# Optimization experiments

Measured on AMD Instinct MI355X. Metric: run time of the kernel, lower is better.

## Reference

```python
import jax, jax.numpy as jnp
import numpy as np

EPSILON = 1e-15
CUTOFF = 5.0
N_RBF = 16           # num_radial_filters -> RBF dim = 2*16+1 = 33
SCALE = 8            # _quadrature_points_per_atom_scaling


def poly_envelope_5_2(x):
    # e3nn.poly_envelope(5, 2): f'(x) ~ x^5 (1-x)^2, f(0)=1, f(1)=0
    x2 = x * x
    x6 = x2 * x2 * x2
    f = 1.0 - 28.0 * x6 + 48.0 * x6 * x - 21.0 * x6 * x2
    return jnp.where(x < 1.0, f, jnp.zeros_like(x))


def sin_cos_basis(r, n_rbf):
    r = r[..., None]                                  # [A,T,1]
    k = jnp.arange(1, n_rbf + 1, dtype=r.dtype)       # [n_rbf]
    return jnp.sqrt(2.0) * jnp.concatenate(
        [0.1 * jnp.ones_like(r), jnp.sin(k * jnp.pi * r), jnp.cos(k * jnp.pi * r)],
        axis=-1,
    )                                                 # [A,T,2*n_rbf+1]


def spherical_harmonics_l012_norm(d):
    # Real spherical harmonics up to l=2, e3nn m-ordering, normalization='norm'
    # (each l-block has unit norm for unit input directions).
    x, y, z = d[..., 0], d[..., 1], d[..., 2]
    r2 = x * x + y * y + z * z
    s3 = jnp.sqrt(3.0)
    one = jnp.ones_like(x)
    return jnp.stack(
        [
            one,                       # l=0
            y, z, x,                   # l=1 (m=-1,0,1)
            s3 * x * y,                # l=2 m=-2
            s3 * y * z,                # l=2 m=-1
            0.5 * (3.0 * z * z - r2),  # l=2 m=0
            s3 * x * z,                # l=2 m=1
            0.5 * s3 * (x * x - y * y) # l=2 m=2
        ],
        axis=-1,
    )                                  # [A,T,9]


def setup_inputs() -> dict:
    key = jax.random.key(0)
    k1, k2, k3, k4 = jax.random.split(key, 4)
    A, N = 64, 200000
    nuc_pos = 4.0 * jax.random.normal(k1, (A, 3), dtype=jnp.float32)
    grid_coords = 4.0 * jax.random.normal(k2, (N, 3), dtype=jnp.float32)
    weights = jax.random.uniform(k3, (N,), dtype=jnp.float32)
    n = jax.random.uniform(k4, (N,), dtype=jnp.float32)
    atom_mask = jnp.ones((A,), dtype=bool)
    return {"nuc_pos": nuc_pos, "atom_mask": atom_mask,
            "grid_coords": grid_coords, "weights": weights, "n": n}


def reference(nuc_pos, atom_mask, grid_coords, weights, n):
    g = grid_coords / CUTOFF                          # [N,3]
    p = nuc_pos / CUTOFF                              # [A,3]
    diff = p[:, None] - g[None]                       # [A,N,3]
    dist = jnp.linalg.norm(diff, axis=-1)             # [A,N]
    A, N = dist.shape
    T = min(N, SCALE * N // A)                        # static
    idx = jnp.argsort(dist, axis=1)[:, :T]            # [A,T] nearest grid points
    diff = jnp.take_along_axis(diff, idx[:, :, None], axis=1)   # [A,T,3]
    dist = jnp.take_along_axis(dist, idx, axis=1)                # [A,T]
    n_t = n[idx]                                      # [A,T]
    w_t = weights[idx]                                # [A,T]
    rbf = sin_cos_basis(dist, N_RBF) * poly_envelope_5_2(dist)[..., None]  # [A,T,33]
    dirs = diff / (dist[..., None] + EPSILON)         # [A,T,3]
    sh = spherical_harmonics_l012_norm(dirs)          # [A,T,9]
    node_feats = jnp.einsum('atr,ath,at,at->arh', rbf, sh, n_t, w_t)  # [A,33,9]
    return node_feats
```

## Files before the change

### kernel.cpp

```cpp
#include <hip/hip_runtime.h>
#include <hip/hip_fp16.h>


typedef float f32x4 __attribute__((ext_vector_type(4)));
typedef int   i32x4 __attribute__((ext_vector_type(4)));

#define SLICES 32
#define NB1    256
#define NB2    512
#define CLAMP0 4000u
#define CHA    1
#define NCHUNK (SLICES * CHA)
#define PBSTR  304
#define CUT25  0x41C80000u
#define WROWS  49
#define BBASE  (33 * 72)

__device__ __forceinline__ unsigned short tobf(float v) {
  return (unsigned short)((__float_as_uint(v) + 0x8000u) >> 16);
}

__device__ __forceinline__ unsigned pack2h(float a, float b) {
  __half2 h = __floats2half2_rn(a, b);
  return *reinterpret_cast<unsigned*>(&h);
}

__device__ __forceinline__ void mfma_acc(f32x4& d, i32x4 a, i32x4 b) {
  asm("v_mfma_f32_16x16x32_bf16 %0, %1, %2, %0" : "+v"(d) : "v"(a), "v"(b));
}

__global__ __launch_bounds__(256) void enc_hist_store(
    const float* __restrict__ nuc, const float* __restrict__ grid,
    const float* __restrict__ wv, const float* __restrict__ nv, int N,
    unsigned* __restrict__ hists, unsigned* __restrict__ cnt,
    unsigned* __restrict__ bitsArr, uint2* __restrict__ pay, int scap,
    unsigned* __restrict__ ghist2) {
  __shared__ unsigned lh[NB1];
  __shared__ unsigned s_cnt;
  int a = blockIdx.x / SLICES, s = blockIdx.x % SLICES;
  int tid = threadIdx.x, lane = tid & 63;
  if (tid < NB1) lh[tid] = 0;
  if (tid == 0) s_cnt = 0;
  {
    const int stripe = NB2 / SLICES;
    if (tid < stripe) ghist2[(size_t)a * NB2 + s * stripe + tid] = 0;
  }
  __syncthreads();

  float px = nuc[3*a+0], py = nuc[3*a+1], pz = nuc[3*a+2];
  unsigned* segb = bitsArr + (size_t)blockIdx.x * scap;
  uint2*    segp = pay     + (size_t)blockIdx.x * scap;
  const float4* G4 = (const float4*)grid;
  const float4* W4 = (const float4*)wv;
  const float4* V4 = (const float4*)nv;
  int nq = N >> 2;
  int qper = (nq + SLICES - 1) / SLICES;
  int qlo = s * qper, qhi = min(nq, qlo + qper);

  for (int qi = qlo + tid; qi < qhi; qi += 256) {
    float4 A4 = G4[3*qi], B4 = G4[3*qi+1], C4 = G4[3*qi+2];
    float4 w4 = W4[qi], v4 = V4[qi];
    float xs[4] = {A4.x, A4.w, B4.z, C4.y};
    float ys[4] = {A4.y, B4.x, B4.w, C4.z};
    float zs[4] = {A4.z, B4.y, C4.x, C4.w};
    float nws[4] = {v4.x * w4.x, v4.y * w4.y, v4.z * w4.z, v4.w * w4.w};
    float dxs[4], dys[4], dzs[4];
    unsigned bt[4];
    #pragma unroll
    for (int k = 0; k < 4; ++k) {
      float dx = px - xs[k], dy = py - ys[k], dz = pz - zs[k];
      dxs[k] = dx; dys[k] = dy; dzs[k] = dz;
      float d2 = __fmaf_rn(dx, dx, __fmaf_rn(dy, dy, __fmul_rn(dz, dz)));
      bt[k] = __float_as_uint(d2);
      if (bt[k] < CUT25) {
        int cb = (int)(bt[k] >> 18) - (int)CLAMP0;
        atomicAdd(&lh[cb > 0 ? cb : 0], 1u);
      }
    }
    #pragma unroll
    for (int k = 0; k < 4; ++k) {
      bool sel = bt[k] < CUT25;
      unsigned long long mm = __ballot(sel);
      if (mm) {
        int leader = __ffsll(mm) - 1;
        unsigned base = 0;
        if (lane == leader) base = atomicAdd(&s_cnt, (unsigned)__popcll(mm));
        base = __shfl(base, leader);
        if (sel) {
          unsigned pos = base + (unsigned)__popcll(mm & ((1ull << lane) - 1ull));
          if (pos < (unsigned)scap) {
            segb[pos] = bt[k];
            segp[pos] = make_uint2(pack2h(dxs[k], dys[k]), pack2h(dzs[k], nws[k]));
          }
        }
      }
    }
  }
  if (s == SLICES - 1) {
    for (int i = 4*nq + tid; i < N; i += 256) {
      float dx = px - grid[3*i+0], dy = py - grid[3*i+1], dz = pz - grid[3*i+2];
      float d2 = __fmaf_rn(dx, dx, __fmaf_rn(dy, dy, __fmul_rn(dz, dz)));
      unsigned bits = __float_as_uint(d2);
      bool sel = bits < CUT25;
      if (sel) {
        int cb = (int)(bits >> 18) - (int)CLAMP0;
        atomicAdd(&lh[cb > 0 ? cb : 0], 1u);
      }
      unsigned long long mm = __ballot(sel);
      if (mm) {
        int leader = __ffsll(mm) - 1;
        unsigned base = 0;
        if (lane == leader) base = atomicAdd(&s_cnt, (unsigned)__popcll(mm));
        base = __shfl(base, leader);
        if (sel) {
          unsigned pos = base + (unsigned)__popcll(mm & ((1ull << lane) - 1ull));
          if (pos < (unsigned)scap) {
            segb[pos] = bits;
            segp[pos] = make_uint2(pack2h(dx, dy), pack2h(dz, nv[i] * wv[i]));
          }
        }
      }
    }
  }
  __syncthreads();
  if (tid < NB1) hists[(size_t)blockIdx.x * NB1 + tid] = lh[tid];
  if (tid == 0) cnt[blockIdx.x] = s_cnt;
}

__global__ __launch_bounds__(256) void enc_scan1(
    const unsigned* __restrict__ hists, unsigned T,
    unsigned* __restrict__ b1r, unsigned* __restrict__ r2r) {
  __shared__ unsigned lh[NB1];
  __shared__ unsigned s_bin, s_pre;
  int a = blockIdx.x, tid = threadIdx.x;
  if (tid < NB1) {
    unsigned acc = 0;
    const unsigned* base = hists + (size_t)a * SLICES * NB1 + tid;
    #pragma unroll 8
    for (int t = 0; t < SLICES; ++t) acc += base[(size_t)t * NB1];
    lh[tid] = acc;
  }
  if (tid == 0) { s_bin = NB1 - 1; s_pre = 0; }
  __syncthreads();
  if (tid < 64) {
    int lane = tid, base = 4 * lane;
    unsigned h0 = lh[base], h1 = lh[base+1], h2 = lh[base+2], h3 = lh[base+3];
    unsigned ssum = h0 + h1 + h2 + h3;
    unsigned p = ssum;
    #pragma unroll
    for (int d = 1; d < 64; d <<= 1) {
      unsigned t = __shfl_up(p, d);
      if (lane >= d) p += t;
    }
    unsigned excl = p - ssum;
    if (excl < T && T <= p) {
      unsigned cum = excl;
      unsigned hh[4] = {h0, h1, h2, h3};
      #pragma unroll
      for (int k = 0; k < 4; ++k) {
        if (cum + hh[k] >= T) { s_bin = (unsigned)(base + k); s_pre = cum; break; }
        cum += hh[k];
      }
    }
  }
  __syncthreads();
  if (tid == 0) { b1r[a] = s_bin; r2r[a] = T - s_pre; }
}

__global__ __launch_bounds__(256) void enc_fine(
    const unsigned* __restrict__ b1r, const unsigned* __restrict__ cnt,
    const unsigned* __restrict__ bitsArr, int scap,
    unsigned* __restrict__ ghist2) {
  int seg_id = blockIdx.x;
  int a = seg_id / SLICES;
  unsigned b1c = b1r[a];
  unsigned tb1 = b1c + CLAMP0;
  int total = min((int)cnt[seg_id], scap);
  const unsigned* segb = bitsArr + (size_t)seg_id * scap;
  unsigned* gh2 = ghist2 + (size_t)a * NB2;
  for (int i = threadIdx.x; i < total; i += 256) {
    unsigned bits = segb[i];
    unsigned cb = bits >> 18;
    bool match = b1c ? (cb == tb1) : (cb <= CLAMP0);
    if (match) atomicAdd(&gh2[(bits >> 9) & (NB2 - 1)], 1u);
  }
}

__global__ __launch_bounds__(256) void enc_scan2(
    const unsigned* __restrict__ ghist2, const unsigned* __restrict__ b1r,
    const unsigned* __restrict__ r2r, unsigned* __restrict__ thr) {
  __shared__ unsigned lh2[NB2];
  __shared__ unsigned s_bin2;
  int a = blockIdx.x, tid = threadIdx.x;
  const unsigned* gh2 = ghist2 + (size_t)a * NB2;
  lh2[tid] = gh2[tid];
  lh2[tid + 256] = gh2[tid + 256];
  if (tid == 0) s_bin2 = NB2 - 1;
  __syncthreads();
  unsigned R = r2r[a];
  if (tid < 64) {
    int lane = tid, base = 8 * lane;
    unsigned hh[8], ssum = 0;
    #pragma unroll
    for (int k = 0; k < 8; ++k) { hh[k] = lh2[base + k]; ssum += hh[k]; }
    unsigned p = ssum;
    #pragma unroll
    for (int d = 1; d < 64; d <<= 1) {
      unsigned t = __shfl_up(p, d);
      if (lane >= d) p += t;
    }
    unsigned excl = p - ssum;
    if (excl < R && R <= p) {
      unsigned cum = excl;
      #pragma unroll
      for (int k = 0; k < 8; ++k) {
        if (cum + hh[k] >= R) { s_bin2 = (unsigned)(base + k); break; }
        cum += hh[k];
      }
    }
  }
  __syncthreads();
  if (tid == 0) thr[a] = ((b1r[a] + CLAMP0) << 9) | s_bin2;
}

__global__ __launch_bounds__(256, 5) void enc_accum(
    const unsigned* __restrict__ thrv, const unsigned* __restrict__ cnt,
    const unsigned* __restrict__ bitsArr, const uint2* __restrict__ pay,
    int scap, float* __restrict__ pb) {
  __shared__ __align__(16) unsigned short lds[4][WROWS * 72];
  int seg_id = blockIdx.x;
  int a = seg_id / SLICES;
  int tid = threadIdx.x, lane = tid & 63, w = tid >> 6;
  unsigned short* SB = &lds[w][0];

  {
    i32x4 z = {0, 0, 0, 0};
    i32x4* zp = (i32x4*)SB;
    #pragma unroll
    for (int t = 0; t < 7; ++t) {
      int idx = lane + t * 64;
      if (idx < (WROWS * 72) / 8) zp[idx] = z;
    }
  }

  unsigned thr = thrv[a];
  int total = min((int)cnt[seg_id], scap);
  const unsigned* lstb = bitsArr + (size_t)seg_id * scap;
  const uint2*    lstp = pay     + (size_t)seg_id * scap;

  f32x4 acc0 = {0,0,0,0}, acc1 = {0,0,0,0}, acc2 = {0,0,0,0};
  int m = lane & 15, q = lane >> 4;
  const float SQRT2 = 1.41421356237309515f;
  const float PIF   = 3.14159265358979323846f;
  const float S3    = 1.73205080756887729f;

  int j0 = w * 64 + lane;
  unsigned bitsN = (j0 < total) ? lstb[j0] : 0xFFFFFFFFu;
  uint2 prN = make_uint2(0u, 0u);
  if (j0 < total) prN = lstp[j0];

  for (int jb = w * 64; jb < total; jb += 256) {
    unsigned bits = bitsN;
    uint2 pr = prN;
    int jn = jb + 256 + lane;
    if (jn < total) { bitsN = lstb[jn]; prN = lstp[jn]; }
    bool live = (jb + lane < total) && ((bits >> 9) <= thr);
    if (live) {
      float d2 = __uint_as_float(bits);
      __half2 hxy = *reinterpret_cast<const __half2*>(&pr.x);
      __half2 hzn = *reinterpret_cast<const __half2*>(&pr.y);
      float dx = __low2float(hxy), dy = __high2float(hxy);
      float dz = __low2float(hzn), nw = __high2float(hzn);
#if __has_builtin(__builtin_amdgcn_sqrtf)
      float rn = __builtin_amdgcn_sqrtf(d2) * 0.2f;
#else
      float rn = sqrtf(d2) * 0.2f;
#endif
      float x2 = rn * rn;
      float x6 = x2 * x2 * x2;
      float e  = __fmaf_rn(x6, __fmaf_rn(-21.f, x2, __fmaf_rn(48.f, rn, -28.f)), 1.f);
      float f  = SQRT2 * e;
#if __has_builtin(__builtin_amdgcn_rcpf)
      float inv = 0.2f * __builtin_amdgcn_rcpf(rn + 1e-15f);
#else
      float inv = 0.2f / (rn + 1e-15f);
#endif
      float X = dx * inv, Y = dy * inv, Z = dz * inv;
      float r2 = __fmaf_rn(X, X, __fmaf_rn(Y, Y, Z * Z));
      SB[BBASE + 0*72 + lane] = tobf(nw);
      SB[BBASE + 1*72 + lane] = tobf(nw * Y);
      SB[BBASE + 2*72 + lane] = tobf(nw * Z);
      SB[BBASE + 3*72 + lane] = tobf(nw * X);
      SB[BBASE + 4*72 + lane] = tobf(nw * S3 * X * Y);
      SB[BBASE + 5*72 + lane] = tobf(nw * S3 * Y * Z);
      SB[BBASE + 6*72 + lane] = tobf(nw * 0.5f * __fmaf_rn(3.f, Z * Z, -r2));
      SB[BBASE + 7*72 + lane] = tobf(nw * S3 * X * Z);
      SB[BBASE + 8*72 + lane] = tobf(nw * 0.5f * S3 * (X * X - Y * Y));
      float s1, c1;
      __sincosf(PIF * rn, &s1, &c1);
      SB[0 * 72 + lane]  = tobf(0.1f * f);
      float sk = s1, ck = c1;
      SB[1 * 72 + lane]  = tobf(f * sk);
      SB[17 * 72 + lane] = tobf(f * ck);
      #pragma unroll
      for (int k = 2; k <= 16; ++k) {
        float sn = __fmaf_rn(sk, c1, ck * s1);
        float cn = __fmaf_rn(ck, c1, -(sk * s1));
        sk = sn; ck = cn;
        SB[k * 72 + lane]        = tobf(f * sk);
        SB[(16 + k) * 72 + lane] = tobf(f * ck);
      }
    } else {
      #pragma unroll
      for (int h = 0; h < 9; ++h) SB[BBASE + h * 72 + lane] = 0;
    }
    #pragma unroll
    for (int g = 0; g < 2; ++g) {
      int cb = 8 * q + 32 * g;
      i32x4 bf = *(const i32x4*)&SB[BBASE + m * 72 + cb];
      i32x4 a0 = *(const i32x4*)&SB[(0  + m) * 72 + cb];
      mfma_acc(acc0, a0, bf);
      i32x4 a1 = *(const i32x4*)&SB[(16 + m) * 72 + cb];
      mfma_acc(acc1, a1, bf);
      i32x4 a2 = *(const i32x4*)&SB[(32 + m) * 72 + cb];
      mfma_acc(acc2, a2, bf);
    }
  }
  asm volatile("s_nop 7\n\ts_nop 7" : "+v"(acc0), "+v"(acc1), "+v"(acc2));

  float* redw = (float*)&lds[w][0];
  if (m < 9) {
    #pragma unroll
    for (int t = 0; t < 4; ++t) {
      int row = 4 * q + t;
      redw[(row +  0) * 9 + m] = acc0[t];
      redw[(row + 16) * 9 + m] = acc1[t];
      if (row + 32 < 33) redw[(row + 32) * 9 + m] = acc2[t];
    }
  }
  __syncthreads();
  float* pbb = pb + (size_t)blockIdx.x * PBSTR;
  for (int v = tid; v < 297; v += 256) {
    float s0 = ((const float*)&lds[0][0])[v] + ((const float*)&lds[1][0])[v];
    float s1 = ((const float*)&lds[2][0])[v] + ((const float*)&lds[3][0])[v];
    pbb[v] = s0 + s1;
  }
}

__global__ __launch_bounds__(256) void enc_reduce(
    const float* __restrict__ pb, float* __restrict__ out, int nout) {
  int idx = blockIdx.x * 256 + threadIdx.x;
  if (idx >= nout) return;
  int a = idx / 297, v = idx - a * 297;
  const float* p = pb + (size_t)a * NCHUNK * PBSTR + v;
  float s = 0.f;
  #pragma unroll 8
  for (int k = 0; k < NCHUNK; ++k) s += p[(size_t)k * PBSTR];
  out[idx] = s;
}

extern "C" void kernel_launch(void* const* d_in, const int* in_sizes, int n_in,
                              void* d_out, int out_size, void* d_ws, size_t ws_size,
                              hipStream_t stream) {
  const float* nuc  = (const float*)d_in[0];
  const float* grid = (const float*)d_in[2];
  const float* wts  = (const float*)d_in[3];
  const float* nn   = (const float*)d_in[4];
  int A = in_sizes[0] / 3;
  int N = in_sizes[2] / 3;
  long long t8 = (8LL * (long long)N) / (long long)A;
  unsigned T = (unsigned)(t8 < (long long)N ? t8 : (long long)N);

  unsigned* ws      = (unsigned*)d_ws;
  unsigned* cnt     = ws;
  unsigned* b1r     = cnt + A * SLICES;
  unsigned* r2r     = b1r + A;
  unsigned* thr     = r2r + A;
  unsigned* hists   = thr + A;
  unsigned* ghist2  = hists + (size_t)A * SLICES * NB1;
  float*    pb      = (float*)(ghist2 + (size_t)A * NB2);
  unsigned* bitsArr = (unsigned*)(pb + (size_t)A * SLICES * CHA * PBSTR);

  int nq   = N >> 2;
  int qper = (nq + SLICES - 1) / SLICES;
  int SCAP = qper * 4 + 4;
  {
    long long head  = (long long)(bitsArr - ws);
    long long avail = (long long)(ws_size / 4) - head;
    long long need  = 3LL * SCAP * A * SLICES;
    if (avail > 0 && need > avail) SCAP = (int)(avail / (3LL * A * SLICES));
    SCAP &= ~1;
  }
  uint2* pay = (uint2*)(bitsArr + (size_t)A * SLICES * SCAP);
  float* out = (float*)d_out;
  int nout = A * 297;

  enc_hist_store<<<A * SLICES,         256, 0, stream>>>(nuc, grid, wts, nn, N, hists,
                                                         cnt, bitsArr, pay, SCAP, ghist2);
  enc_scan1     <<<A,                  256, 0, stream>>>(hists, T, b1r, r2r);
  enc_fine      <<<A * SLICES,         256, 0, stream>>>(b1r, cnt, bitsArr, SCAP, ghist2);
  enc_scan2     <<<A,                  256, 0, stream>>>(ghist2, b1r, r2r, thr);
  enc_accum     <<<A * SLICES * CHA,   256, 0, stream>>>(thr, cnt, bitsArr, pay, SCAP, pb);
  enc_reduce    <<<(nout + 255) / 256, 256, 0, stream>>>(pb, out, nout);
}
```

Before: 57.52 us.

## Process four atoms per block in histogram/store pass to reuse grid loads

After: 65.57 us. 14.0% more time.

```diff
diff --git a/kernel.cpp b/kernel.cpp
--- a/kernel.cpp
+++ b/kernel.cpp
@@ -6,11 +6,11 @@
 typedef int   i32x4 __attribute__((ext_vector_type(4)));
 
 #define SLICES 32
+#define AG     4
 #define NB1    256
 #define NB2    512
 #define CLAMP0 4000u
-#define CHA    1
-#define NCHUNK (SLICES * CHA)
+#define NCHUNK SLICES
 #define PBSTR  304
 #define CUT25  0x41C80000u
 #define WROWS  49
@@ -35,21 +35,41 @@
     unsigned* __restrict__ hists, unsigned* __restrict__ cnt,
     unsigned* __restrict__ bitsArr, uint2* __restrict__ pay, int scap,
     unsigned* __restrict__ ghist2) {
-  __shared__ unsigned lh[NB1];
-  __shared__ unsigned s_cnt;
-  int a = blockIdx.x / SLICES, s = blockIdx.x % SLICES;
+  __shared__ unsigned lh[AG][NB1];
+  __shared__ unsigned s_cnt[AG];
+  int ag = blockIdx.x / SLICES, s = blockIdx.x % SLICES;
+  int a0 = ag * AG;
   int tid = threadIdx.x, lane = tid & 63;
-  if (tid < NB1) lh[tid] = 0;
-  if (tid == 0) s_cnt = 0;
+  if (tid < NB1) {
+    #pragma unroll
+    for (int aa = 0; aa < AG; ++aa) lh[aa][tid] = 0;
+  }
+  if (tid < AG) s_cnt[tid] = 0;
   {
     const int stripe = NB2 / SLICES;
-    if (tid < stripe) ghist2[(size_t)a * NB2 + s * stripe + tid] = 0;
-  }
-  __syncthreads();
-
-  float px = nuc[3*a+0], py = nuc[3*a+1], pz = nuc[3*a+2];
-  unsigned* segb = bitsArr + (size_t)blockIdx.x * scap;
-  uint2*    segp = pay     + (size_t)blockIdx.x * scap;
+    if (tid < stripe) {
+      #pragma unroll
+      for (int aa = 0; aa < AG; ++aa)
+        ghist2[(size_t)(a0 + aa) * NB2 + s * stripe + tid] = 0;
+    }
+  }
+  __syncthreads();
+
+  float pxs[AG], pys[AG], pzs[AG];
+  #pragma unroll
+  for (int aa = 0; aa < AG; ++aa) {
+    pxs[aa] = nuc[3*(a0+aa)+0];
+    pys[aa] = nuc[3*(a0+aa)+1];
+    pzs[aa] = nuc[3*(a0+aa)+2];
+  }
+  unsigned* segb[AG];
+  uint2*    segp[AG];
+  #pragma unroll
+  for (int aa = 0; aa < AG; ++aa) {
+    size_t off = (size_t)((a0 + aa) * SLICES + s) * scap;
+    segb[aa] = bitsArr + off;
+    segp[aa] = pay + off;
+  }
   const float4* G4 = (const float4*)grid;
   const float4* W4 = (const float4*)wv;
   const float4* V4 = (const float4*)nv;
@@ -64,33 +84,38 @@
     float ys[4] = {A4.y, B4.x, B4.w, C4.z};
     float zs[4] = {A4.z, B4.y, C4.x, C4.w};
     float nws[4] = {v4.x * w4.x, v4.y * w4.y, v4.z * w4.z, v4.w * w4.w};
-    float dxs[4], dys[4], dzs[4];
-    unsigned bt[4];
-    #pragma unroll
-    for (int k = 0; k < 4; ++k) {
-      float dx = px - xs[k], dy = py - ys[k], dz = pz - zs[k];
-      dxs[k] = dx; dys[k] = dy; dzs[k] = dz;
-      float d2 = __fmaf_rn(dx, dx, __fmaf_rn(dy, dy, __fmul_rn(dz, dz)));
-      bt[k] = __float_as_uint(d2);
-      if (bt[k] < CUT25) {
-        int cb = (int)(bt[k] >> 18) - (int)CLAMP0;
-        atomicAdd(&lh[cb > 0 ? cb : 0], 1u);
-      }
-    }
-    #pragma unroll
-    for (int k = 0; k < 4; ++k) {
-      bool sel = bt[k] < CUT25;
-      unsigned long long mm = __ballot(sel);
-      if (mm) {
-        int leader = __ffsll(mm) - 1;
-        unsigned base = 0;
-        if (lane == leader) base = atomicAdd(&s_cnt, (unsigned)__popcll(mm));
-        base = __shfl(base, leader);
-        if (sel) {
-          unsigned pos = base + (unsigned)__popcll(mm & ((1ull << lane) - 1ull));
-          if (pos < (unsigned)scap) {
-            segb[pos] = bt[k];
-            segp[pos] = make_uint2(pack2h(dxs[k], dys[k]), pack2h(dzs[k], nws[k]));
+    #pragma unroll
+    for (int aa = 0; aa < AG; ++aa) {
+      float px = pxs[aa], py = pys[aa], pz = pzs[aa];
+      float dxs[4], dys[4], dzs[4];
+      unsigned bt[4];
+      #pragma unroll
+      for (int k = 0; k < 4; ++k) {
+        float dx = px - xs[k], dy = py - ys[k], dz = pz - zs[k];
+        dxs[k] = dx; dys[k] = dy; dzs[k] = dz;
+        float d2 = __fmaf_rn(dx, dx, __fmaf_rn(dy, dy, __fmul_rn(dz, dz)));
+        bt[k] = __float_as_uint(d2);
+        if (bt[k] < CUT25) {
+          int cb = (int)(bt[k] >> 18) - (int)CLAMP0;
+          atomicAdd(&lh[aa][cb > 0 ? cb : 0], 1u);
+        }
+      }
+      #pragma unroll
+      for (int k = 0; k < 4; ++k) {
+        bool sel = bt[k] < CUT25;
+        unsigned long long mm = __ballot(sel);
+        if (mm) {
+          int leader = __ffsll(mm) - 1;
+          unsigned base = 0;
+          if (lane == leader) base = atomicAdd(&s_cnt[aa], (unsigned)__popcll(mm));
+          base = __shfl(base, leader);
+          if (sel) {
+            unsigned pos = base + (unsigned)__popcll(mm & ((1ull << lane) - 1ull));
+            if (pos < (unsigned)scap) {
+              segb[aa][pos] = bt[k];
+              segp[aa][pos] = make_uint2(pack2h(dxs[k], dys[k]),
+                                         pack2h(dzs[k], nws[k]));
+            }
           }
         }
       }
@@ -98,33 +123,42 @@
   }
   if (s == SLICES - 1) {
     for (int i = 4*nq + tid; i < N; i += 256) {
-      float dx = px - grid[3*i+0], dy = py - grid[3*i+1], dz = pz - grid[3*i+2];
-      float d2 = __fmaf_rn(dx, dx, __fmaf_rn(dy, dy, __fmul_rn(dz, dz)));
-      unsigned bits = __float_as_uint(d2);
-      bool sel = bits < CUT25;
-      if (sel) {
-        int cb = (int)(bits >> 18) - (int)CLAMP0;
-        atomicAdd(&lh[cb > 0 ? cb : 0], 1u);
-      }
-      unsigned long long mm = __ballot(sel);
-      if (mm) {
-        int leader = __ffsll(mm) - 1;
-        unsigned base = 0;
-        if (lane == leader) base = atomicAdd(&s_cnt, (unsigned)__popcll(mm));
-        base = __shfl(base, leader);
+      float gx = grid[3*i+0], gy = grid[3*i+1], gz = grid[3*i+2];
+      float nwi = nv[i] * wv[i];
+      #pragma unroll
+      for (int aa = 0; aa < AG; ++aa) {
+        float dx = pxs[aa] - gx, dy = pys[aa] - gy, dz = pzs[aa] - gz;
+        float d2 = __fmaf_rn(dx, dx, __fmaf_rn(dy, dy, __fmul_rn(dz, dz)));
+        unsigned bits = __float_as_uint(d2);
+        bool sel = bits < CUT25;
         if (sel) {
-          unsigned pos = base + (unsigned)__popcll(mm & ((1ull << lane) - 1ull));
-          if (pos < (unsigned)scap) {
-            segb[pos] = bits;
-            segp[pos] = make_uint2(pack2h(dx, dy), pack2h(dz, nv[i] * wv[i]));
+          int cb = (int)(bits >> 18) - (int)CLAMP0;
+          atomicAdd(&lh[aa][cb > 0 ? cb : 0], 1u);
+        }
+        unsigned long long mm = __ballot(sel);
+        if (mm) {
+          int leader = __ffsll(mm) - 1;
+          unsigned base = 0;
+          if (lane == leader) base = atomicAdd(&s_cnt[aa], (unsigned)__popcll(mm));
+          base = __shfl(base, leader);
+          if (sel) {
+            unsigned pos = base + (unsigned)__popcll(mm & ((1ull << lane) - 1ull));
+            if (pos < (unsigned)scap) {
+              segb[aa][pos] = bits;
+              segp[aa][pos] = make_uint2(pack2h(dx, dy), pack2h(dz, nwi));
+            }
           }
         }
       }
     }
   }
   __syncthreads();
-  if (tid < NB1) hists[(size_t)blockIdx.x * NB1 + tid] = lh[tid];
-  if (tid == 0) cnt[blockIdx.x] = s_cnt;
+  if (tid < NB1) {
+    #pragma unroll
+    for (int aa = 0; aa < AG; ++aa)
+      hists[(size_t)((a0 + aa) * SLICES + s) * NB1 + tid] = lh[aa][tid];
+  }
+  if (tid < AG) cnt[(a0 + tid) * SLICES + s] = s_cnt[tid];
 }
 
 __global__ __launch_bounds__(256) void enc_scan1(
@@ -379,7 +413,7 @@
   unsigned* hists   = thr + A;
   unsigned* ghist2  = hists + (size_t)A * SLICES * NB1;
   float*    pb      = (float*)(ghist2 + (size_t)A * NB2);
-  unsigned* bitsArr = (unsigned*)(pb + (size_t)A * SLICES * CHA * PBSTR);
+  unsigned* bitsArr = (unsigned*)(pb + (size_t)A * NCHUNK * PBSTR);
 
   int nq   = N >> 2;
   int qper = (nq + SLICES - 1) / SLICES;
@@ -395,11 +429,11 @@
   float* out = (float*)d_out;
   int nout = A * 297;
 
-  enc_hist_store<<<A * SLICES,         256, 0, stream>>>(nuc, grid, wts, nn, N, hists,
+  enc_hist_store<<<(A / AG) * SLICES,  256, 0, stream>>>(nuc, grid, wts, nn, N, hists,
                                                          cnt, bitsArr, pay, SCAP, ghist2);
   enc_scan1     <<<A,                  256, 0, stream>>>(hists, T, b1r, r2r);
   enc_fine      <<<A * SLICES,         256, 0, stream>>>(b1r, cnt, bitsArr, SCAP, ghist2);
   enc_scan2     <<<A,                  256, 0, stream>>>(ghist2, b1r, r2r, thr);
-  enc_accum     <<<A * SLICES * CHA,   256, 0, stream>>>(thr, cnt, bitsArr, pay, SCAP, pb);
+  enc_accum     <<<A * SLICES,         256, 0, stream>>>(thr, cnt, bitsArr, pay, SCAP, pb);
   enc_reduce    <<<(nout + 255) / 256, 256, 0, stream>>>(pb, out, nout);
 }
```
